# Performance work log

Measured on AMD Instinct MI355X. Metric: run time of the kernel, lower is better.

## Reference

```python
import jax, jax.numpy as jnp
import numpy as np

NEG_BIG = -1e10  # K.switch(A==0, -1e10, 0) mask value
LRELU_ALPHA = 0.2


def setup_inputs() -> dict:
    key = jax.random.key(0)
    kX, kA, kW, kS, kN = jax.random.split(key, 5)
    B, N, F, H, F_ = 4, 2048, 256, 8, 64
    X = jax.random.normal(kX, (B, N, F), dtype=jnp.float32)
    A = jax.random.bernoulli(kA, 0.05, (B, N, N)).astype(jnp.float32)
    eye = jnp.eye(N, dtype=jnp.float32)[None]
    A = jnp.maximum(A, eye)
    W = jax.random.normal(kW, (H, F, F_), dtype=jnp.float32) * 0.05
    a_self = jax.random.normal(kS, (H, F_), dtype=jnp.float32) * 0.05
    a_neigh = jax.random.normal(kN, (H, F_), dtype=jnp.float32) * 0.05
    return {"X": X, "A": A, "W": W, "a_self": a_self, "a_neigh": a_neigh}


def reference(X, A, W, a_self, a_neigh):
    # per-head linear transform, vectorized over heads: [B,H,N,F_]
    h = jnp.einsum('bnf,hfo->bhno', X, W)
    att_s = jnp.einsum('bhno,ho->bhn', h, a_self)    # attn_for_self
    att_n = jnp.einsum('bhno,ho->bhn', h, a_neigh)   # attn_for_neighs
    # broadcast-add -> dense NxN scores per head, LeakyReLU(0.2)
    dense = att_s[:, :, :, None] + att_n[:, :, None, :]          # [B,H,N,N]
    dense = jax.nn.leaky_relu(dense, LRELU_ALPHA)
    mask = jnp.where(A == 0.0, NEG_BIG, 0.0)[:, None, :, :]      # [B,1,N,N]
    attn = jax.nn.softmax(dense + mask, axis=-1)
    # weighted aggregation (dropout is identity at inference / attn_dropout=0)
    out = jnp.einsum('bhnm,bhmo->bhno', attn, h)                 # [B,H,N,F_]
    out = jax.nn.relu(out)                                       # per-head activation (concat mode)
    B, H, N, F_ = out.shape
    return out.transpose(0, 2, 1, 3).reshape(B, N, H * F_)       # concat heads
```

## Files before the change

### kernel.cpp

```cpp
#include <hip/hip_runtime.h>


constexpr int GN  = 2048;
constexpr int GHF = 512;

using sh8    = __attribute__((ext_vector_type(8))) short;
using us4g   = __attribute__((ext_vector_type(4))) unsigned short;
using f32x4g = __attribute__((ext_vector_type(4))) float;
using u32x4g = __attribute__((ext_vector_type(4))) unsigned int;
using i32x4g = __attribute__((ext_vector_type(4))) int;

__device__ inline float gat_bf2f(unsigned short u) {
    union { unsigned int i; float f; } c; c.i = ((unsigned int)u) << 16; return c.f;
}
__device__ inline unsigned short gat_f2bf(float f) {
    union { float f; unsigned int i; } c; c.f = f;
    return (unsigned short)((c.i + 0x7fffu + ((c.i >> 16) & 1u)) >> 16);
}
__device__ inline int gat_isf32(const float* __restrict__ Aw) {
    float a = Aw[0];
    return (a == 0.0f) || (a == 1.0f);
}
__device__ inline unsigned int gat_enc(float f) {
    union { float f; unsigned int u; } c; c.f = f;
    return (c.u & 0x80000000u) ? ~c.u : (c.u | 0x80000000u);
}
__device__ inline float gat_dec(unsigned int e) {
    union { float f; unsigned int u; } c;
    c.u = (e & 0x80000000u) ? (e & 0x7fffffffu) : ~e;
    return c.f;
}
__device__ inline size_t gat_hswz_idx(int o, int j) {
    int jc = j >> 5, quad = (j >> 3) & 3, e = j & 7;
    int lane = quad * 16 + (o & 15);
    return (((size_t)(jc * 4 + (o >> 4))) * 64 + lane) * 8 + e;
}

__global__ void GraphAttention_62981400429165_kernel() {}

constexpr size_t OFF_HS   = 256;
constexpr size_t OFF_ATTS = OFF_HS   + 8388608;
constexpr size_t OFF_TB   = OFF_ATTS + 262144;
constexpr size_t OFF_MASK = OFF_TB   + 262144;
constexpr size_t OFF_MAXN = OFF_MASK + 2097152;
constexpr size_t OFF_XC   = OFF_MAXN + 256;
constexpr size_t OFF_WC   = OFF_XC   + 4194304;

__global__ __launch_bounds__(256) void k_mask_conv(const void* __restrict__ Araw,
                                                   const void* __restrict__ Xraw,
                                                   const void* __restrict__ Wraw,
                                                   unsigned long long* __restrict__ mask,
                                                   unsigned int* __restrict__ maxn_enc,
                                                   unsigned short* __restrict__ Xc,
                                                   unsigned short* __restrict__ Wc) {
    int tid = threadIdx.x, blk = blockIdx.x;
    int isf = gat_isf32((const float*)Araw);
    if (blk < 65536) {
        if (blk == 0 && tid < 32) maxn_enc[tid] = 0u;
        size_t idx = (size_t)blk * 256 + tid;
        int nz;
        if (isf) nz = (((const float*)Araw)[idx] != 0.0f);
        else     nz = (((const unsigned short*)Araw)[idx] != 0);
        unsigned long long bal = __ballot(nz);
        if ((tid & 63) == 0) mask[idx >> 6] = bal;
    } else if (blk < 73728) {
        int i = (blk - 65536) * 256 + tid;
        Xc[i] = isf ? gat_f2bf(((const float*)Xraw)[i]) : ((const unsigned short*)Xraw)[i];
    } else {
        int i = (blk - 73728) * 256 + tid;
        Wc[i] = isf ? gat_f2bf(((const float*)Wraw)[i]) : ((const unsigned short*)Wraw)[i];
    }
}

constexpr int LDW = 264;
__global__ __launch_bounds__(256) void k_gemm1(const unsigned short* __restrict__ Xc,
                                               const unsigned short* __restrict__ Wc,
                                               const void* __restrict__ aSraw,
                                               const void* __restrict__ aNraw,
                                               const float* __restrict__ Aw,
                                               unsigned short* __restrict__ hswz,
                                               float* __restrict__ att_s,
                                               unsigned int* __restrict__ Tb,
                                               unsigned int* __restrict__ maxn_enc) {
    int blk = blockIdx.x;
    int bh = blk >> 3, it = blk & 7;
    int b = bh >> 3, hh = bh & 7;
    int isf = gat_isf32(Aw);
    __shared__ unsigned short Wt[64 * LDW];
    for (int idx = threadIdx.x; idx < 256 * 64; idx += 256) {
        int k = idx >> 6, col = idx & 63;
        Wt[col * LDW + k] = Wc[(hh * 256 + k) * 64 + col];
    }
    __syncthreads();
#if defined(__gfx950__)
    int wave = threadIdx.x >> 6, lane = threadIdx.x & 63;
    int lrw = lane & 15, quad = lane >> 4;
    int row0 = it * 256 + wave * 64;
    f32x4g acc[4][4] = {};
    for (int k0 = 0; k0 < 256; k0 += 32) {
        sh8 a[4], w[4];
        for (int rt = 0; rt < 4; rt++)
            a[rt] = *(const sh8*)&Xc[((size_t)(b * GN) + row0 + rt * 16 + lrw) * 256 + k0 + quad * 8];
        for (int ct = 0; ct < 4; ct++)
            w[ct] = *(const sh8*)&Wt[(ct * 16 + lrw) * LDW + k0 + quad * 8];
        for (int rt = 0; rt < 4; rt++)
            for (int ct = 0; ct < 4; ct++)
                acc[rt][ct] = __builtin_amdgcn_mfma_f32_16x16x32_bf16(a[rt], w[ct], acc[rt][ct], 0, 0, 0);
    }
    float as_l[4], an_l[4];
    for (int ct = 0; ct < 4; ct++) {
        int col = hh * 64 + ct * 16 + lrw;
        as_l[ct] = isf ? ((const float*)aSraw)[col] : gat_bf2f(((const unsigned short*)aSraw)[col]);
        an_l[ct] = isf ? ((const float*)aNraw)[col] : gat_bf2f(((const unsigned short*)aNraw)[col]);
    }
    float wmax = -3e38f;
    for (int rt = 0; rt < 4; rt++)
        for (int r = 0; r < 4; r++) {
            float ps = acc[rt][0][r] * as_l[0] + acc[rt][1][r] * as_l[1]
                     + acc[rt][2][r] * as_l[2] + acc[rt][3][r] * as_l[3];
            float pn = acc[rt][0][r] * an_l[0] + acc[rt][1][r] * an_l[1]
                     + acc[rt][2][r] * an_l[2] + acc[rt][3][r] * an_l[3];
            for (int off = 1; off < 16; off <<= 1) {
                ps += __shfl_xor(ps, off);
                pn += __shfl_xor(pn, off);
            }
            int row = row0 + rt * 16 + quad * 4 + r;
            if (lrw == 0) {
                att_s[bh * GN + row] = ps;
                Tb[bh * GN + row] = ((unsigned int)gat_f2bf(__expf(pn)) << 16)
                                  | (unsigned int)gat_f2bf(__expf(0.2f * pn));
            }
            wmax = fmaxf(wmax, pn);
        }
    wmax = fmaxf(wmax, __shfl_xor(wmax, 16));
    wmax = fmaxf(wmax, __shfl_xor(wmax, 32));
    if (lane == 0) atomicMax(&maxn_enc[bh], gat_enc(wmax));
    __syncthreads();
    unsigned short* CtT = Wt;
    for (int rt = 0; rt < 4; rt++)
        for (int ct = 0; ct < 4; ct++) {
            int o = ct * 16 + lrw;
            int nloc = wave * 64 + rt * 16 + quad * 4;
            us4g v;
            v[0] = gat_f2bf(acc[rt][ct][0]);
            v[1] = gat_f2bf(acc[rt][ct][1]);
            v[2] = gat_f2bf(acc[rt][ct][2]);
            v[3] = gat_f2bf(acc[rt][ct][3]);
            *(us4g*)&CtT[o * LDW + nloc] = v;
        }
    __syncthreads();
    for (int k = 0; k < 8; k++) {
        int id = k * 256 + threadIdx.x;
        int ln = id & 63, t = id >> 6;
        int jc_loc = t >> 2, ct = t & 3;
        int lrw2 = ln & 15, quad2 = ln >> 4;
        int o = ct * 16 + lrw2;
        int nloc = jc_loc * 32 + quad2 * 8;
        sh8 v = *(const sh8*)&CtT[o * LDW + nloc];
        size_t dst = ((((size_t)(bh * 64 + it * 8 + jc_loc)) * 4 + ct) * 64 + ln) * 8;
        *(sh8*)&hswz[dst] = v;
    }
#else
    int row = it * 256 + threadIdx.x;
    float hrow[64];
    for (int col = 0; col < 64; col++) {
        float s = 0.f;
        for (int k = 0; k < 256; k++)
            s += gat_bf2f(Xc[((size_t)(b * GN) + row) * 256 + k]) * gat_bf2f(Wt[col * LDW + k]);
        hrow[col] = s;
        hswz[(size_t)bh * 64 * GN * 2 / 2 * 0 + 0] = hswz[0];
    }
    for (int col = 0; col < 64; col++) {
        size_t base = (size_t)bh * 64 * GN;
        hswz[base + gat_hswz_idx(col, row)] = gat_f2bf(hrow[col]);
    }
    float ps = 0.f, pn = 0.f;
    for (int col = 0; col < 64; col++) {
        float as = isf ? ((const float*)aSraw)[hh * 64 + col] : gat_bf2f(((const unsigned short*)aSraw)[hh * 64 + col]);
        float an = isf ? ((const float*)aNraw)[hh * 64 + col] : gat_bf2f(((const unsigned short*)aNraw)[hh * 64 + col]);
        ps += hrow[col] * as;
        pn += hrow[col] * an;
    }
    att_s[bh * GN + row] = ps;
    Tb[bh * GN + row] = ((unsigned int)gat_f2bf(__expf(pn)) << 16)
                      | (unsigned int)gat_f2bf(__expf(0.2f * pn));
    atomicMax(&maxn_enc[bh], gat_enc(pn));
#endif
}

__global__ __launch_bounds__(128, 4) void k_attn_av(const unsigned int* __restrict__ mask32,
                                                    const unsigned short* __restrict__ hswz,
                                                    const float* __restrict__ att_s,
                                                    const unsigned int* __restrict__ Tb,
                                                    const unsigned int* __restrict__ maxn_enc,
                                                    const float* __restrict__ Aw,
                                                    void* __restrict__ outv) {
    int blk = blockIdx.x;
    int bh = blk & 31, it = blk >> 5;
    int b = bh >> 3, hh = bh & 7;
    int i0 = it * 32;
    int tid = threadIdx.x;
    int isf = gat_isf32(Aw);
    float maxn = gat_dec(maxn_enc[bh]);
    const unsigned int* Tp = Tb + (size_t)bh * GN;
#if defined(__gfx950__)
    int wave = tid >> 6, lane = tid & 63, lrw = lane & 15, quad = lane >> 4;
    int kq = quad * 8;
    int j0 = wave * 1024;
    const unsigned short* hs = hswz + ((size_t)(bh * 64) + wave * 32) * 2048 + lane * 8;
    float k1[2], k2[2], T0[2];
    const unsigned int* mrf[2];
    for (int f = 0; f < 2; f++) {
        int row = i0 + f * 16 + lrw;
        float s = att_s[bh * GN + row];
        float z = s + maxn;
        float c = fmaxf(z, 0.2f * z);
        k1[f] = __expf(s - c);
        k2[f] = __expf(0.2f * s - c);
        T0[f] = __expf(-s);
        mrf[f] = mask32 + ((size_t)(b * GN) + row) * 64 + wave * 32;
    }
    f32x4g acc[2][4] = {};
    f32x4g accl[2] = {};
    sh8 ones;
#pragma unroll
    for (int e = 0; e < 8; e++) ones[e] = (short)0x3f80;

#pragma unroll 1
    for (int jg = 0; jg < 8; jg++) {
        u32x4g m0 = *(const u32x4g*)&mrf[0][jg * 4];
        u32x4g m1 = *(const u32x4g*)&mrf[1][jg * 4];
#pragma unroll
        for (int sj = 0; sj < 4; sj++) {
            int jc = jg * 4 + sj;
            int jq = j0 + jc * 32 + kq;
            u32x4g tA = *(const u32x4g*)&Tp[jq];
            u32x4g tB = *(const u32x4g*)&Tp[jq + 4];
            const unsigned short* hp = hs + jc * 2048;
            sh8 b0 = *(const sh8*)&hp[0];
            sh8 b1 = *(const sh8*)&hp[512];
            sh8 b2 = *(const sh8*)&hp[1024];
            sh8 b3 = *(const sh8*)&hp[1536];
            unsigned int w0 = m0[sj] >> kq;
            unsigned int w1 = m1[sj] >> kq;
            unsigned int q0[8], q1[8];
#pragma unroll
            for (int e = 0; e < 8; e++) {
                unsigned int word = (e < 4) ? tA[e] : tB[e - 4];
                float Ev  = __uint_as_float(word & 0xffff0000u);
                float E5v = __uint_as_float(word << 16);
                float p0 = (Ev > T0[0]) ? (k1[0] * Ev) : (k2[0] * E5v);
                float p1 = (Ev > T0[1]) ? (k1[1] * Ev) : (k2[1] * E5v);
                p0 = ((w0 >> e) & 1u) ? p0 : 0.0f;
                p1 = ((w1 >> e) & 1u) ? p1 : 0.0f;
                q0[e] = __float_as_uint(p0);
                q1[e] = __float_as_uint(p1);
            }
            i32x4g f0, f1;
#pragma unroll
            for (int pp = 0; pp < 4; pp++) {
                f0[pp] = (int)((q0[2 * pp] >> 16) | (q0[2 * pp + 1] & 0xffff0000u));
                f1[pp] = (int)((q1[2 * pp] >> 16) | (q1[2 * pp + 1] & 0xffff0000u));
            }
            sh8 af0 = *(sh8*)&f0;
            sh8 af1 = *(sh8*)&f1;
            acc[0][0] = __builtin_amdgcn_mfma_f32_16x16x32_bf16(af0, b0, acc[0][0], 0, 0, 0);
            acc[1][0] = __builtin_amdgcn_mfma_f32_16x16x32_bf16(af1, b0, acc[1][0], 0, 0, 0);
            acc[0][1] = __builtin_amdgcn_mfma_f32_16x16x32_bf16(af0, b1, acc[0][1], 0, 0, 0);
            acc[1][1] = __builtin_amdgcn_mfma_f32_16x16x32_bf16(af1, b1, acc[1][1], 0, 0, 0);
            acc[0][2] = __builtin_amdgcn_mfma_f32_16x16x32_bf16(af0, b2, acc[0][2], 0, 0, 0);
            acc[1][2] = __builtin_amdgcn_mfma_f32_16x16x32_bf16(af1, b2, acc[1][2], 0, 0, 0);
            acc[0][3] = __builtin_amdgcn_mfma_f32_16x16x32_bf16(af0, b3, acc[0][3], 0, 0, 0);
            acc[1][3] = __builtin_amdgcn_mfma_f32_16x16x32_bf16(af1, b3, acc[1][3], 0, 0, 0);
            accl[0] = __builtin_amdgcn_mfma_f32_16x16x32_bf16(af0, ones, accl[0], 0, 0, 0);
            accl[1] = __builtin_amdgcn_mfma_f32_16x16x32_bf16(af1, ones, accl[1], 0, 0, 0);
        }
    }
    __shared__ float lred[2 * 32];
    __shared__ float lsum[32];
    __shared__ float red[2 * 2 * 16 * 17];
    if (lrw == 0) {
#pragma unroll
        for (int f = 0; f < 2; f++)
#pragma unroll
            for (int r = 0; r < 4; r++)
                lred[wave * 32 + f * 16 + quad * 4 + r] = accl[f][r];
    }
    __syncthreads();
    if (tid < 32)
        lsum[tid] = 1.0f / (lred[tid] + lred[32 + tid]);
    __syncthreads();
    for (int ct = 0; ct < 4; ct++) {
#pragma unroll
        for (int f = 0; f < 2; f++)
#pragma unroll
            for (int r = 0; r < 4; r++)
                red[wave * 544 + f * 272 + (quad * 4 + r) * 17 + lrw] = acc[f][ct][r];
        __syncthreads();
#pragma unroll
        for (int k = 0; k < 4; k++) {
            int pos = k * 128 + tid;
            int f = pos >> 8, r16 = (pos >> 4) & 15, c16 = pos & 15;
            int bse = f * 272 + r16 * 17 + c16;
            float sum = red[bse] + red[bse + 544];
            float v = sum * lsum[f * 16 + r16];
            v = v > 0.f ? v : 0.f;
            int row = i0 + f * 16 + r16;
            size_t o = ((size_t)(b * GN) + row) * GHF + hh * 64 + ct * 16 + c16;
            if (isf) ((float*)outv)[o] = v;
            else     ((unsigned short*)outv)[o] = gat_f2bf(v);
        }
        __syncthreads();
    }
#else
    int row = i0 + (tid >> 2), chh = (tid & 3) * 16;
    const unsigned short* hbb = hswz + (size_t)(bh * 64) * GN;
    const unsigned int* mr = mask32 + ((size_t)(b * GN) + row) * 64;
    float s = att_s[bh * GN + row];
    float z = s + maxn;
    float c = fmaxf(z, 0.2f * z);
    float k1 = __expf(s - c), k2 = __expf(0.2f * s - c), T0 = __expf(-s);
    float l = 0.f;
    float accS[16] = {};
    for (int j = 0; j < GN; j++) {
        if (!((mr[j >> 5] >> (j & 31)) & 1u)) continue;
        unsigned int word = Tp[j];
        float Ev  = __uint_as_float(word & 0xffff0000u);
        float E5v = __uint_as_float(word << 16);
        float p = (Ev > T0) ? (k1 * Ev) : (k2 * E5v);
        union { float f; unsigned int u; } t; t.f = p; t.u &= 0xffff0000u;
        l += t.f;
        for (int cc = 0; cc < 16; cc++)
            accS[cc] += t.f * gat_bf2f(hbb[gat_hswz_idx(chh + cc, j)]);
    }
    float li = 1.0f / l;
    for (int cc = 0; cc < 16; cc++) {
        float v = accS[cc] * li; v = v > 0.f ? v : 0.f;
        size_t oi = ((size_t)(b * GN) + row) * GHF + hh * 64 + chh + cc;
        if (isf) ((float*)outv)[oi] = v;
        else     ((unsigned short*)outv)[oi] = gat_f2bf(v);
    }
#endif
}

extern "C" void kernel_launch(void* const* d_in, const int* in_sizes, int n_in,
                              void* d_out, int out_size, void* d_ws, size_t ws_size,
                              hipStream_t stream) {
    const void* X  = d_in[0];
    const void* A  = d_in[1];
    const void* W  = d_in[2];
    const void* aS = d_in[3];
    const void* aN = d_in[4];

    char* ws = (char*)d_ws;
    unsigned short* hswz = (unsigned short*)(ws + OFF_HS);
    float* att_s = (float*)(ws + OFF_ATTS);
    unsigned int* Tb = (unsigned int*)(ws + OFF_TB);
    unsigned long long* mask = (unsigned long long*)(ws + OFF_MASK);
    unsigned int* maxn_enc = (unsigned int*)(ws + OFF_MAXN);
    unsigned short* Xc = (unsigned short*)(ws + OFF_XC);
    unsigned short* Wc = (unsigned short*)(ws + OFF_WC);

    k_mask_conv<<<74240, 256, 0, stream>>>(A, X, W, mask, maxn_enc, Xc, Wc);
    k_gemm1<<<256, 256, 0, stream>>>(Xc, Wc, aS, aN, (const float*)A,
                                     hswz, att_s, Tb, maxn_enc);
    k_attn_av<<<2048, 128, 0, stream>>>((const unsigned int*)mask, hswz,
                                        att_s, Tb, maxn_enc,
                                        (const float*)A, d_out);
}
```

Baseline: 199.9 us.

## Pre-swizzle X into MFMA layout, vectorize conversion, and double GEMM1 grid

The prep kernel now handles four elements per thread for the mask ballot and for the X/W bf16 conversion, using vector loads and far fewer blocks. It writes X directly in the MFMA operand-tile layout so GEMM1 can load fragments contiguously. GEMM1 uses 128-row tiles per block, giving a grid of 512 blocks for more parallelism, at the cost of reloading W into LDS twice as often. The attention kernel replaces the threshold compare plus select for LeakyReLU-exp with a fmaxf of the two candidates, which drops one exp per row.

```diff
diff --git a/kernel.cpp b/kernel.cpp
--- a/kernel.cpp
+++ b/kernel.cpp
@@ -35,6 +35,10 @@
     int lane = quad * 16 + (o & 15);
     return (((size_t)(jc * 4 + (o >> 4))) * 64 + lane) * 8 + e;
 }
+__device__ inline size_t gat_xswz_idx(int bn, int k) {
+    return ((((size_t)(bn >> 4)) * 8 + (k >> 5)) * 64
+            + ((k >> 3) & 3) * 16 + (bn & 15)) * 8 + (k & 7);
+}
 
 __global__ void GraphAttention_62981400429165_kernel() {}
 
@@ -43,37 +47,59 @@
 constexpr size_t OFF_TB   = OFF_ATTS + 262144;
 constexpr size_t OFF_MASK = OFF_TB   + 262144;
 constexpr size_t OFF_MAXN = OFF_MASK + 2097152;
-constexpr size_t OFF_XC   = OFF_MAXN + 256;
-constexpr size_t OFF_WC   = OFF_XC   + 4194304;
+constexpr size_t OFF_XS   = OFF_MAXN + 256;
+constexpr size_t OFF_WC   = OFF_XS   + 4194304;
 
 __global__ __launch_bounds__(256) void k_mask_conv(const void* __restrict__ Araw,
                                                    const void* __restrict__ Xraw,
                                                    const void* __restrict__ Wraw,
                                                    unsigned long long* __restrict__ mask,
                                                    unsigned int* __restrict__ maxn_enc,
-                                                   unsigned short* __restrict__ Xc,
+                                                   unsigned short* __restrict__ Xswz,
                                                    unsigned short* __restrict__ Wc) {
     int tid = threadIdx.x, blk = blockIdx.x;
     int isf = gat_isf32((const float*)Araw);
-    if (blk < 65536) {
+    if (blk < 16384) {
         if (blk == 0 && tid < 32) maxn_enc[tid] = 0u;
-        size_t idx = (size_t)blk * 256 + tid;
-        int nz;
-        if (isf) nz = (((const float*)Araw)[idx] != 0.0f);
-        else     nz = (((const unsigned short*)Araw)[idx] != 0);
-        unsigned long long bal = __ballot(nz);
-        if ((tid & 63) == 0) mask[idx >> 6] = bal;
-    } else if (blk < 73728) {
-        int i = (blk - 65536) * 256 + tid;
-        Xc[i] = isf ? gat_f2bf(((const float*)Xraw)[i]) : ((const unsigned short*)Xraw)[i];
+        int wv = tid >> 6, ln = tid & 63;
+        size_t base = (size_t)blk * 1024 + wv * 256;
+#pragma unroll
+        for (int e = 0; e < 4; e++) {
+            size_t idx = base + e * 64 + ln;
+            int nz;
+            if (isf) nz = (((const float*)Araw)[idx] != 0.0f);
+            else     nz = (((const unsigned short*)Araw)[idx] != 0);
+            unsigned long long bal = __ballot(nz);
+            if (ln == 0) mask[blk * 16 + wv * 4 + e] = bal;
+        }
+    } else if (blk < 18432) {
+        int i = (blk - 16384) * 1024 + tid * 4;
+        int bn = i >> 8, k = i & 255;
+        us4g v;
+        if (isf) {
+            f32x4g x = *(const f32x4g*)&((const float*)Xraw)[i];
+            v[0] = gat_f2bf(x[0]); v[1] = gat_f2bf(x[1]);
+            v[2] = gat_f2bf(x[2]); v[3] = gat_f2bf(x[3]);
+        } else {
+            v = *(const us4g*)&((const unsigned short*)Xraw)[i];
+        }
+        *(us4g*)&Xswz[gat_xswz_idx(bn, k)] = v;
     } else {
-        int i = (blk - 73728) * 256 + tid;
-        Wc[i] = isf ? gat_f2bf(((const float*)Wraw)[i]) : ((const unsigned short*)Wraw)[i];
+        int i = (blk - 18432) * 1024 + tid * 4;
+        us4g v;
+        if (isf) {
+            f32x4g x = *(const f32x4g*)&((const float*)Wraw)[i];
+            v[0] = gat_f2bf(x[0]); v[1] = gat_f2bf(x[1]);
+            v[2] = gat_f2bf(x[2]); v[3] = gat_f2bf(x[3]);
+        } else {
+            v = *(const us4g*)&((const unsigned short*)Wraw)[i];
+        }
+        *(us4g*)&Wc[i] = v;
     }
 }
 
 constexpr int LDW = 264;
-__global__ __launch_bounds__(256) void k_gemm1(const unsigned short* __restrict__ Xc,
+__global__ __launch_bounds__(256) void k_gemm1(const unsigned short* __restrict__ Xswz,
                                                const unsigned short* __restrict__ Wc,
                                                const void* __restrict__ aSraw,
                                                const void* __restrict__ aNraw,
@@ -83,7 +109,7 @@
                                                unsigned int* __restrict__ Tb,
                                                unsigned int* __restrict__ maxn_enc) {
     int blk = blockIdx.x;
-    int bh = blk >> 3, it = blk & 7;
+    int bh = blk >> 4, it = blk & 15;
     int b = bh >> 3, hh = bh & 7;
     int isf = gat_isf32(Aw);
     __shared__ unsigned short Wt[64 * LDW];
@@ -95,15 +121,16 @@
 #if defined(__gfx950__)
     int wave = threadIdx.x >> 6, lane = threadIdx.x & 63;
     int lrw = lane & 15, quad = lane >> 4;
-    int row0 = it * 256 + wave * 64;
-    f32x4g acc[4][4] = {};
-    for (int k0 = 0; k0 < 256; k0 += 32) {
-        sh8 a[4], w[4];
-        for (int rt = 0; rt < 4; rt++)
-            a[rt] = *(const sh8*)&Xc[((size_t)(b * GN) + row0 + rt * 16 + lrw) * 256 + k0 + quad * 8];
+    int row0 = it * 128 + wave * 32;
+    int tile0 = b * 128 + (row0 >> 4);
+    f32x4g acc[2][4] = {};
+    for (int kt = 0; kt < 8; kt++) {
+        sh8 a[2], w[4];
+        for (int rt = 0; rt < 2; rt++)
+            a[rt] = *(const sh8*)&Xswz[((((size_t)(tile0 + rt)) * 8 + kt) * 64 + lane) * 8];
         for (int ct = 0; ct < 4; ct++)
-            w[ct] = *(const sh8*)&Wt[(ct * 16 + lrw) * LDW + k0 + quad * 8];
-        for (int rt = 0; rt < 4; rt++)
+            w[ct] = *(const sh8*)&Wt[(ct * 16 + lrw) * LDW + kt * 32 + quad * 8];
+        for (int rt = 0; rt < 2; rt++)
             for (int ct = 0; ct < 4; ct++)
                 acc[rt][ct] = __builtin_amdgcn_mfma_f32_16x16x32_bf16(a[rt], w[ct], acc[rt][ct], 0, 0, 0);
     }
@@ -114,7 +141,7 @@
         an_l[ct] = isf ? ((const float*)aNraw)[col] : gat_bf2f(((const unsigned short*)aNraw)[col]);
     }
     float wmax = -3e38f;
-    for (int rt = 0; rt < 4; rt++)
+    for (int rt = 0; rt < 2; rt++)
         for (int r = 0; r < 4; r++) {
             float ps = acc[rt][0][r] * as_l[0] + acc[rt][1][r] * as_l[1]
                      + acc[rt][2][r] * as_l[2] + acc[rt][3][r] * as_l[3];
@@ -137,10 +164,10 @@
     if (lane == 0) atomicMax(&maxn_enc[bh], gat_enc(wmax));
     __syncthreads();
     unsigned short* CtT = Wt;
-    for (int rt = 0; rt < 4; rt++)
+    for (int rt = 0; rt < 2; rt++)
         for (int ct = 0; ct < 4; ct++) {
             int o = ct * 16 + lrw;
-            int nloc = wave * 64 + rt * 16 + quad * 4;
+            int nloc = wave * 32 + rt * 16 + quad * 4;
             us4g v;
             v[0] = gat_f2bf(acc[rt][ct][0]);
             v[1] = gat_f2bf(acc[rt][ct][1]);
@@ -149,7 +176,7 @@
             *(us4g*)&CtT[o * LDW + nloc] = v;
         }
     __syncthreads();
-    for (int k = 0; k < 8; k++) {
+    for (int k = 0; k < 4; k++) {
         int id = k * 256 + threadIdx.x;
         int ln = id & 63, t = id >> 6;
         int jc_loc = t >> 2, ct = t & 3;
@@ -157,34 +184,35 @@
         int o = ct * 16 + lrw2;
         int nloc = jc_loc * 32 + quad2 * 8;
         sh8 v = *(const sh8*)&CtT[o * LDW + nloc];
-        size_t dst = ((((size_t)(bh * 64 + it * 8 + jc_loc)) * 4 + ct) * 64 + ln) * 8;
+        size_t dst = ((((size_t)(bh * 64 + it * 4 + jc_loc)) * 4 + ct) * 64 + ln) * 8;
         *(sh8*)&hswz[dst] = v;
     }
 #else
-    int row = it * 256 + threadIdx.x;
-    float hrow[64];
-    for (int col = 0; col < 64; col++) {
-        float s = 0.f;
-        for (int k = 0; k < 256; k++)
-            s += gat_bf2f(Xc[((size_t)(b * GN) + row) * 256 + k]) * gat_bf2f(Wt[col * LDW + k]);
-        hrow[col] = s;
-        hswz[(size_t)bh * 64 * GN * 2 / 2 * 0 + 0] = hswz[0];
-    }
-    for (int col = 0; col < 64; col++) {
+    if (threadIdx.x < 128) {
+        int row = it * 128 + threadIdx.x;
+        int bn = b * GN + row;
+        float hrow[64];
+        for (int col = 0; col < 64; col++) {
+            float s = 0.f;
+            for (int k = 0; k < 256; k++)
+                s += gat_bf2f(Xswz[gat_xswz_idx(bn, k)]) * gat_bf2f(Wt[col * LDW + k]);
+            hrow[col] = s;
+        }
         size_t base = (size_t)bh * 64 * GN;
-        hswz[base + gat_hswz_idx(col, row)] = gat_f2bf(hrow[col]);
-    }
-    float ps = 0.f, pn = 0.f;
-    for (int col = 0; col < 64; col++) {
-        float as = isf ? ((const float*)aSraw)[hh * 64 + col] : gat_bf2f(((const unsigned short*)aSraw)[hh * 64 + col]);
-        float an = isf ? ((const float*)aNraw)[hh * 64 + col] : gat_bf2f(((const unsigned short*)aNraw)[hh * 64 + col]);
-        ps += hrow[col] * as;
-        pn += hrow[col] * an;
-    }
-    att_s[bh * GN + row] = ps;
-    Tb[bh * GN + row] = ((unsigned int)gat_f2bf(__expf(pn)) << 16)
-                      | (unsigned int)gat_f2bf(__expf(0.2f * pn));
-    atomicMax(&maxn_enc[bh], gat_enc(pn));
+        for (int col = 0; col < 64; col++)
+            hswz[base + gat_hswz_idx(col, row)] = gat_f2bf(hrow[col]);
+        float ps = 0.f, pn = 0.f;
+        for (int col = 0; col < 64; col++) {
+            float as = isf ? ((const float*)aSraw)[hh * 64 + col] : gat_bf2f(((const unsigned short*)aSraw)[hh * 64 + col]);
+            float an = isf ? ((const float*)aNraw)[hh * 64 + col] : gat_bf2f(((const unsigned short*)aNraw)[hh * 64 + col]);
+            ps += hrow[col] * as;
+            pn += hrow[col] * an;
+        }
+        att_s[bh * GN + row] = ps;
+        Tb[bh * GN + row] = ((unsigned int)gat_f2bf(__expf(pn)) << 16)
+                          | (unsigned int)gat_f2bf(__expf(0.2f * pn));
+        atomicMax(&maxn_enc[bh], gat_enc(pn));
+    }
 #endif
 }
 
@@ -208,7 +236,7 @@
     int kq = quad * 8;
     int j0 = wave * 1024;
     const unsigned short* hs = hswz + ((size_t)(bh * 64) + wave * 32) * 2048 + lane * 8;
-    float k1[2], k2[2], T0[2];
+    float k1[2], k2[2];
     const unsigned int* mrf[2];
     for (int f = 0; f < 2; f++) {
         int row = i0 + f * 16 + lrw;
@@ -217,7 +245,6 @@
         float c = fmaxf(z, 0.2f * z);
         k1[f] = __expf(s - c);
         k2[f] = __expf(0.2f * s - c);
-        T0[f] = __expf(-s);
         mrf[f] = mask32 + ((size_t)(b * GN) + row) * 64 + wave * 32;
     }
     f32x4g acc[2][4] = {};
@@ -249,8 +276,8 @@
                 unsigned int word = (e < 4) ? tA[e] : tB[e - 4];
                 float Ev  = __uint_as_float(word & 0xffff0000u);
                 float E5v = __uint_as_float(word << 16);
-                float p0 = (Ev > T0[0]) ? (k1[0] * Ev) : (k2[0] * E5v);
-                float p1 = (Ev > T0[1]) ? (k1[1] * Ev) : (k2[1] * E5v);
+                float p0 = fmaxf(k1[0] * Ev, k2[0] * E5v);
+                float p1 = fmaxf(k1[1] * Ev, k2[1] * E5v);
                 p0 = ((w0 >> e) & 1u) ? p0 : 0.0f;
                 p1 = ((w1 >> e) & 1u) ? p1 : 0.0f;
                 q0[e] = __float_as_uint(p0);
@@ -319,7 +346,7 @@
     float s = att_s[bh * GN + row];
     float z = s + maxn;
     float c = fmaxf(z, 0.2f * z);
-    float k1 = __expf(s - c), k2 = __expf(0.2f * s - c), T0 = __expf(-s);
+    float k1 = __expf(s - c), k2 = __expf(0.2f * s - c);
     float l = 0.f;
     float accS[16] = {};
     for (int j = 0; j < GN; j++) {
@@ -327,7 +354,7 @@
         unsigned int word = Tp[j];
         float Ev  = __uint_as_float(word & 0xffff0000u);
         float E5v = __uint_as_float(word << 16);
-        float p = (Ev > T0) ? (k1 * Ev) : (k2 * E5v);
+        float p = fmaxf(k1 * Ev, k2 * E5v);
         union { float f; unsigned int u; } t; t.f = p; t.u &= 0xffff0000u;
         l += t.f;
         for (int cc = 0; cc < 16; cc++)
@@ -358,11 +385,11 @@
     unsigned int* Tb = (unsigned int*)(ws + OFF_TB);
     unsigned long long* mask = (unsigned long long*)(ws + OFF_MASK);
     unsigned int* maxn_enc = (unsigned int*)(ws + OFF_MAXN);
-    unsigned short* Xc = (unsigned short*)(ws + OFF_XC);
+    unsigned short* Xswz = (unsigned short*)(ws + OFF_XS);
     unsigned short* Wc = (unsigned short*)(ws + OFF_WC);
 
-    k_mask_conv<<<74240, 256, 0, stream>>>(A, X, W, mask, maxn_enc, Xc, Wc);
-    k_gemm1<<<256, 256, 0, stream>>>(Xc, Wc, aS, aN, (const float*)A,
+    k_mask_conv<<<18560, 256, 0, stream>>>(A, X, W, mask, maxn_enc, Xswz, Wc);
+    k_gemm1<<<512, 256, 0, stream>>>(Xswz, Wc, aS, aN, (const float*)A,
                                      hswz, att_s, Tb, maxn_enc);
     k_attn_av<<<2048, 128, 0, stream>>>((const unsigned int*)mask, hswz,
                                         att_s, Tb, maxn_enc,
```

After: 202.4 us. About the same (+1.3%).
